# Optimization experiments

Measured on AMD Instinct MI355X. Metric: run time of the kernel, lower is better.

## Reference

```python
import jax, jax.numpy as jnp
import numpy as np

B = 2            # batch size
GRID = 256       # BEV grid H = W
M = 30000        # number of pillars (voxels)
NPTS = 200000    # number of points
IN_C = 16
VOXEL = 0.4      # voxel_size[:2]
PC_MIN = -51.2   # pc_range[:2]
DS = 2           # prod(ds_layer_strides)


def _bn(x, g, b):
    # eval-mode BatchNorm with running_mean=0, running_var=1 (eps absorbed into g)
    return x * g + b


def _conv(x, k, stride):
    # 3x3 conv, padding=1 (spconv SparseConv2d / SubMConv2d with pad k//2), NHWC
    return jax.lax.conv_general_dilated(
        x, k, (stride, stride), ((1, 1), (1, 1)),
        dimension_numbers=('NHWC', 'HWIO', 'NHWC'))


def _active_mask(occ, stride):
    # active output sites of a sparse conv = any active input in the 3x3 receptive field
    pooled = jax.lax.reduce_window(occ, -jnp.inf, jax.lax.max,
                                   (1, 3, 3, 1), (1, stride, stride, 1),
                                   ((0, 0), (1, 1), (1, 1), (0, 0)))
    return (pooled > 0).astype(occ.dtype)


def _forward(features, pfn_w0, pfn_g0, pfn_b0, pfn_w1, pfn_g1, pfn_b1,
             b1_kd, b1_gd, b1_bd, b1_k1, b1_g1, b1_b1, b1_k2, b1_g2, b1_b2,
             b2_kd, b2_gd, b2_bd, b2_k1, b2_g1, b2_b1, b2_k2, b2_g2, b2_b2,
             unq, unq_inv, grid_size):
    # pillar mode: cols 0:2 are xy; convert to (fractional) voxel coordinates
    pos = (features[:, :2] - PC_MIN) / VOXEL  # [N,2] = (px, py)

    # PFN layer 0 (not last): linear(16->16) + BN + ReLU, concat per-pillar max
    h = jax.nn.relu(_bn(features @ pfn_w0, pfn_g0, pfn_b0))            # [N,16]
    hmax = jax.ops.segment_max(h, unq_inv, num_segments=M)             # [M,16]
    h = jnp.concatenate([h, hmax[unq_inv]], axis=1)                    # [N,32]
    # PFN layer 1 (last): linear(32->64) + BN + ReLU
    h = jax.nn.relu(_bn(h @ pfn_w1, pfn_g1, pfn_b1))                   # [N,64]

    # scatter_max pooling points -> pillars
    fv = jax.ops.segment_max(h, unq_inv, num_segments=M)               # [M,64]

    Hn = grid_size
    img = jnp.zeros((B, Hn, Hn, fv.shape[1]), fv.dtype)
    img = img.at[unq[:, 0], unq[:, 1], unq[:, 2]].set(fv)              # dense BEV, NHWC
    occ = jnp.zeros((B, Hn, Hn, 1), fv.dtype)
    occ = occ.at[unq[:, 0], unq[:, 1], unq[:, 2]].set(1.0)

    # block 1: SparseConvBlock(stride=1) + SparseBasicBlock (dense math, masked to active sites)
    occ1 = _active_mask(occ, 1)
    x = jax.nn.relu(_bn(_conv(img, b1_kd, 1), b1_gd, b1_bd)) * occ1
    y = jax.nn.relu(_bn(_conv(x, b1_k1, 1), b1_g1, b1_b1)) * occ1
    y = _bn(_conv(y, b1_k2, 1), b1_g2, b1_b2) * occ1
    x = jax.nn.relu(x + y)

    # block 2: SparseConvBlock(stride=2) + SparseBasicBlock
    occ2 = _active_mask(occ1, 2)
    x = jax.nn.relu(_bn(_conv(x, b2_kd, 2), b2_gd, b2_bd)) * occ2
    y = jax.nn.relu(_bn(_conv(x, b2_k1, 1), b2_g1, b2_b1)) * occ2
    y = _bn(_conv(y, b2_k2, 1), b2_g2, b2_b2) * occ2
    x = jax.nn.relu(x + y)                                             # [B,H/2,W/2,128]

    # bilinear gather at per-point downsampled positions (px -> W axis, py -> H axis)
    bidx = unq[unq_inv, 0]
    px = pos[:, 0] / DS
    py = pos[:, 1] / DS
    Hc, Wc = x.shape[1], x.shape[2]
    x0 = jnp.clip(jnp.floor(px).astype(jnp.int32), 0, Wc - 1)
    x1 = jnp.clip(jnp.floor(px).astype(jnp.int32) + 1, 0, Wc - 1)
    y0 = jnp.clip(jnp.floor(py).astype(jnp.int32), 0, Hc - 1)
    y1 = jnp.clip(jnp.floor(py).astype(jnp.int32) + 1, 0, Hc - 1)
    Ia = x[bidx, y0, x0]
    Ib = x[bidx, y1, x0]
    Ic = x[bidx, y0, x1]
    Id = x[bidx, y1, x1]
    x0f, x1f = x0.astype(px.dtype), x1.astype(px.dtype)
    y0f, y1f = y0.astype(py.dtype), y1.astype(py.dtype)
    wa = ((x1f - px) * (y1f - py))[:, None]
    wb = ((x1f - px) * (py - y0f))[:, None]
    wc = ((px - x0f) * (y1f - py))[:, None]
    wd = ((px - x0f) * (py - y0f))[:, None]
    return Ia * wa + Ib * wb + Ic * wc + Id * wd                       # [N,128]


def setup_inputs() -> dict:
    rng = np.random.default_rng(0)
    d = {}
    d['features'] = jnp.asarray(rng.standard_normal((NPTS, IN_C)).astype(np.float32))
    # unique voxel coords (batch, y, x)
    lin = rng.choice(B * GRID * GRID, size=M, replace=False)
    d['unq'] = jnp.asarray(np.stack([lin // (GRID * GRID), (lin // GRID) % GRID, lin % GRID], 1).astype(np.int32))
    # every pillar gets at least one point
    d['unq_inv'] = jnp.asarray(np.concatenate([np.arange(M), rng.integers(0, M, NPTS - M)]).astype(np.int32))
    d['grid_size'] = GRID

    def w(*s):
        fan = int(np.prod(s[:-1]))
        return jnp.asarray((rng.standard_normal(s) / np.sqrt(fan)).astype(np.float32))

    def g(c):
        return jnp.asarray((0.5 + 0.5 * rng.random(c)).astype(np.float32))

    def bb(c):
        return jnp.asarray((0.1 * rng.standard_normal(c)).astype(np.float32))

    d['pfn_w0'] = w(IN_C, 16); d['pfn_g0'] = g(16); d['pfn_b0'] = bb(16)
    d['pfn_w1'] = w(32, 64);   d['pfn_g1'] = g(64); d['pfn_b1'] = bb(64)
    d['b1_kd'] = w(3, 3, 64, 64);   d['b1_gd'] = g(64);  d['b1_bd'] = bb(64)
    d['b1_k1'] = w(3, 3, 64, 64);   d['b1_g1'] = g(64);  d['b1_b1'] = bb(64)
    d['b1_k2'] = w(3, 3, 64, 64);   d['b1_g2'] = g(64);  d['b1_b2'] = bb(64)
    d['b2_kd'] = w(3, 3, 64, 128);  d['b2_gd'] = g(128); d['b2_bd'] = bb(128)
    d['b2_k1'] = w(3, 3, 128, 128); d['b2_g1'] = g(128); d['b2_b1'] = bb(128)
    d['b2_k2'] = w(3, 3, 128, 128); d['b2_g2'] = g(128); d['b2_b2'] = bb(128)
    return d


def reference(features, unq, unq_inv, grid_size,
              pfn_w0, pfn_g0, pfn_b0, pfn_w1, pfn_g1, pfn_b1,
              b1_kd, b1_gd, b1_bd, b1_k1, b1_g1, b1_b1, b1_k2, b1_g2, b1_b2,
              b2_kd, b2_gd, b2_bd, b2_k1, b2_g1, b2_b1, b2_k2, b2_g2, b2_b2):
    return _forward(features, pfn_w0, pfn_g0, pfn_b0, pfn_w1, pfn_g1, pfn_b1,
                    b1_kd, b1_gd, b1_bd, b1_k1, b1_g1, b1_b1, b1_k2, b1_g2, b1_b2,
                    b2_kd, b2_gd, b2_bd, b2_k1, b2_g1, b2_b1, b2_k2, b2_g2, b2_b2,
                    unq, unq_inv, grid_size)
```

## Files before the change

### kernel.cpp

```cpp
#include <hip/hip_runtime.h>
#include <hip/hip_bf16.h>

#define NPTS    200000
#define MPIL    30000
#define BATCH   2
#define GRID0   256
#define PCMIN   (-51.2f)
#define VOXEL0  (0.4f)
#define NCHUNK  118

#define SLOT_B  ((size_t)16777216)
#define SLOT_F  ((size_t)33554432)

#define W0F 0
#define W1F 256
#define FB1 9216
#define FB2 156672
#define FB3 304128
#define FB4 451584
#define FB5 746496
#define FB6 1336320

#define WS_FLAG 0
#define WS_OCC8 64
#define WS_OCC1 (64 + 131072)
#define WS_OCC2 (64 + 262144)
#define WS_HMAX 393280
#define WS_CNT  2313280
#define WS_OFF  2433280
#define WS_CUR  2553344
#define WS_IDX  2673344
#define WS_LOC  3473344
#define WS_BS   3593344
#define WS_FX   393344

typedef __attribute__((ext_vector_type(8))) short v8s;
typedef __attribute__((ext_vector_type(4))) float f32x4;

static __device__ __forceinline__ float b2f(__hip_bfloat16 v) { return __bfloat162float(v); }
static __device__ __forceinline__ unsigned short f2bbits(float f) {
    __hip_bfloat16 h = __float2bfloat16(f);
    union { __hip_bfloat16 h; unsigned short u; } cv; cv.h = h; return cv.u;
}
static __device__ __forceinline__ float bits2f(unsigned short h) {
    union { unsigned int u; float f; } c; c.u = ((unsigned int)h) << 16; return c.f;
}
static __device__ __forceinline__ float lo2f(unsigned int u) {
    union { unsigned int u; float f; } c; c.u = u << 16; return c.f;
}
static __device__ __forceinline__ float hi2f(unsigned int u) {
    union { unsigned int u; float f; } c; c.u = u & 0xFFFF0000u; return c.f;
}
static __device__ __forceinline__ unsigned int pack2(float a, float b) {
    return (unsigned int)f2bbits(a) | ((unsigned int)f2bbits(b) << 16);
}
static __device__ __forceinline__ void split2(float a, float b, unsigned int& hi, unsigned int& lo) {
    unsigned short ha = f2bbits(a), hb = f2bbits(b);
    hi = (unsigned int)ha | ((unsigned int)hb << 16);
    float ra = a - bits2f(ha);
    float rb = b - bits2f(hb);
    lo = (unsigned int)f2bbits(ra) | ((unsigned int)f2bbits(rb) << 16);
}

static __device__ __forceinline__ float ldf(const void* p, size_t i, int isb) {
    return isb ? b2f(((const __hip_bfloat16*)p)[i]) : ((const float*)p)[i];
}
static __device__ __forceinline__ float4 ld4(const void* p, size_t i, int isb) {
    if (isb) {
        uint2 r = *(const uint2*)((const __hip_bfloat16*)p + i);
        return make_float4(lo2f(r.x), hi2f(r.x), lo2f(r.y), hi2f(r.y));
    }
    return *(const float4*)((const float*)p + i);
}
static __device__ __forceinline__ void st4(void* p, size_t i, int isb, float4 v) {
    if (isb) {
        uint2 pk; pk.x = pack2(v.x, v.y); pk.y = pack2(v.z, v.w);
        *(uint2*)((__hip_bfloat16*)p + i) = pk;
    } else {
        *(float4*)((float*)p + i) = v;
    }
}
static __device__ __forceinline__ void* actptr(void* ob, int slot, int isb) {
    return (char*)ob + (size_t)slot * (isb ? SLOT_B : SLOT_F);
}
static __device__ __forceinline__ float* wpool(void* ob, int isb) {
    return (float*)((char*)ob + 3 * (isb ? SLOT_B : SLOT_F));
}

__global__ void probe_kernel(const unsigned short* __restrict__ g0, int* __restrict__ flag) {
    if (threadIdx.x == 0 && blockIdx.x == 0) {
        int ok = 1;
        for (int i = 0; i < 8; i++) {
            unsigned short u = g0[i];
            if (u < 0x3E00 || u >= 0x4000) ok = 0;
        }
        *flag = ok;
    }
}

__global__ __launch_bounds__(256) void cvt_kernel(const void* __restrict__ src, void* ob,
                                                  int woff, int n, const int* __restrict__ flag) {
    int isb = *flag;
    int i = blockIdx.x * 256 + threadIdx.x;
    if (i < n) wpool(ob, isb)[woff + i] = ldf(src, i, isb);
}

__global__ __launch_bounds__(256) void wfrag_kernel(const void* __restrict__ src, void* ob,
                                                    int fb_bytes, int CIN, int COUT,
                                                    const int* __restrict__ flag)
{
    const int isb = *flag;
    const int cnt = 9 * CIN * COUT;
    int e = blockIdx.x * 256 + threadIdx.x;
    if (e >= cnt) return;
    int i = e & 7;
    int l = (e >> 3) & 63;
    int f = e >> 9;
    int nbn = COUT >> 4, kcn = CIN >> 5;
    int nb = f % nbn;
    int kc = (f / nbn) % kcn;
    int tap = f / (nbn * kcn);
    int ci = kc * 32 + (l >> 4) * 8 + i;
    int co = nb * 16 + (l & 15);
    float wv = ldf(src, (size_t)(tap * CIN + ci) * COUT + co, isb);
    unsigned short h = f2bbits(wv);
    float rem = wv - bits2f(h);
    short* wh = (short*)((char*)ob + 3 * (isb ? SLOT_B : SLOT_F) + fb_bytes);
    wh[e] = (short)h;
    wh[cnt + e] = (short)f2bbits(rem);
}

__global__ __launch_bounds__(256) void hist_kernel(const int* __restrict__ unq_inv,
                                                   int* __restrict__ cnt)
{
    int n = blockIdx.x * 256 + threadIdx.x;
    if (n < NPTS) atomicAdd(&cnt[unq_inv[n]], 1);
}

__global__ __launch_bounds__(256) void scan1_kernel(const int* __restrict__ cnt,
                                                    int* __restrict__ loc,
                                                    int* __restrict__ bs)
{
    __shared__ int s[256];
    const int tid = threadIdx.x;
    const int i = blockIdx.x * 256 + tid;
    int v = (i < MPIL) ? cnt[i] : 0;
    s[tid] = v;
    __syncthreads();
#pragma unroll
    for (int d = 1; d < 256; d <<= 1) {
        int t = (tid >= d) ? s[tid - d] : 0;
        __syncthreads();
        s[tid] += t;
        __syncthreads();
    }
    if (i < MPIL) loc[i] = s[tid] - v;
    if (tid == 255) bs[blockIdx.x] = s[255];
}

__global__ __launch_bounds__(128) void scan2_kernel(int* __restrict__ bs)
{
    __shared__ int s[NCHUNK];
    const int tid = threadIdx.x;
    for (int i = tid; i < NCHUNK; i += 128) s[i] = bs[i];
    __syncthreads();
    if (tid == 0) {
        int acc = 0;
        for (int i = 0; i < NCHUNK; i++) { int t = s[i]; s[i] = acc; acc += t; }
    }
    __syncthreads();
    for (int i = tid; i < NCHUNK; i += 128) bs[i] = s[i];
}

__global__ __launch_bounds__(256) void scan3_kernel(const int* __restrict__ loc,
                                                    const int* __restrict__ bs,
                                                    int* __restrict__ off,
                                                    int* __restrict__ cur)
{
    int i = blockIdx.x * 256 + threadIdx.x;
    if (i < MPIL) {
        int e = loc[i] + bs[blockIdx.x];
        off[i] = e; cur[i] = e;
    }
    if (i == 0) off[MPIL] = NPTS;
}

__global__ __launch_bounds__(256) void fill_kernel(const int* __restrict__ unq_inv,
                                                   int* __restrict__ cur,
                                                   int* __restrict__ idxarr)
{
    int n = blockIdx.x * 256 + threadIdx.x;
    if (n >= NPTS) return;
    int p = unq_inv[n];
    int s = atomicAdd(&cur[p], 1);
    idxarr[s] = n;
}

__global__ __launch_bounds__(256) void pfn0_kernel(
    const void* __restrict__ feat, void* ob, const void* __restrict__ g0,
    const void* __restrict__ b0, const int* __restrict__ flag)
{
    const int isb = *flag;
    int n = blockIdx.x * 256 + threadIdx.x;
    if (n >= NPTS) return;
    const float* w0f = wpool(ob, isb) + W0F;
    void* h0 = actptr(ob, 1, isb);
    float f[16];
#pragma unroll
    for (int i = 0; i < 16; i += 4) {
        float4 v = ld4(feat, (size_t)n * 16 + i, isb);
        f[i] = v.x; f[i + 1] = v.y; f[i + 2] = v.z; f[i + 3] = v.w;
    }
#pragma unroll
    for (int co = 0; co < 16; co += 4) {
        float a0 = 0.f, a1 = 0.f, a2 = 0.f, a3 = 0.f;
#pragma unroll
        for (int ci = 0; ci < 16; ci++) {
            float4 w = *(const float4*)&w0f[ci * 16 + co];
            a0 += f[ci] * w.x; a1 += f[ci] * w.y; a2 += f[ci] * w.z; a3 += f[ci] * w.w;
        }
        float o[4] = { a0, a1, a2, a3 };
#pragma unroll
        for (int k = 0; k < 4; k++) {
            float z = o[k] * ldf(g0, co + k, isb) + ldf(b0, co + k, isb);
            o[k] = fmaxf(z, 0.f);
        }
        st4(h0, (size_t)n * 16 + co, isb, make_float4(o[0], o[1], o[2], o[3]));
    }
}

__global__ __launch_bounds__(256) void hmax_kernel(
    void* ob, const int* __restrict__ off, const int* __restrict__ idxarr,
    float* __restrict__ hmax, const int* __restrict__ flag)
{
    const int isb = *flag;
    int t = blockIdx.x * 256 + threadIdx.x;
    if (t >= MPIL * 16) return;
    int p = t >> 4, ch = t & 15;
    const void* h0 = actptr(ob, 1, isb);
    float m = 0.f;
    int s1 = off[p + 1];
    for (int s = off[p]; s < s1; s++) {
        int n = idxarr[s];
        m = fmaxf(m, ldf(h0, (size_t)n * 16 + ch, isb));
    }
    hmax[t] = m;
}

template<bool BF>
static __device__ __forceinline__ void pfn1p_body(
    void* ob, const float* __restrict__ hmax, const void* __restrict__ g1,
    const void* __restrict__ b1, const int* __restrict__ off,
    const int* __restrict__ idxarr, const int* __restrict__ unq,
    unsigned char* __restrict__ occ)
{
    const int lane = threadIdx.x & 63;
    const int p = (blockIdx.x << 2) + (threadIdx.x >> 6);
    if (p >= MPIL) return;
    const int isb = BF ? 1 : 0;
    const float* w1f = wpool(ob, isb) + W1F;
    const void* h0 = actptr(ob, 1, isb);
    void* img = actptr(ob, 0, isb);

    float wcol[32];
#pragma unroll
    for (int k = 0; k < 32; k++) wcol[k] = w1f[k * 64 + lane];
    float base = 0.f;
#pragma unroll
    for (int k = 0; k < 16; k++) base += hmax[(size_t)p * 16 + k] * wcol[16 + k];
    const float g = ldf(g1, lane, isb);
    const float be = ldf(b1, lane, isb);

    float m = 0.f;
    const int s1 = off[p + 1];
    for (int s = off[p]; s < s1; s++) {
        const int n = idxarr[s];
        float h[16];
        if (BF) {
            const unsigned short* hp = (const unsigned short*)h0 + (size_t)n * 16;
            uint4 a = *(const uint4*)hp;
            uint4 c = *(const uint4*)(hp + 8);
            h[0] = lo2f(a.x); h[1] = hi2f(a.x); h[2] = lo2f(a.y); h[3] = hi2f(a.y);
            h[4] = lo2f(a.z); h[5] = hi2f(a.z); h[6] = lo2f(a.w); h[7] = hi2f(a.w);
            h[8] = lo2f(c.x); h[9] = hi2f(c.x); h[10] = lo2f(c.y); h[11] = hi2f(c.y);
            h[12] = lo2f(c.z); h[13] = hi2f(c.z); h[14] = lo2f(c.w); h[15] = hi2f(c.w);
        } else {
            const float* fp = (const float*)h0 + (size_t)n * 16;
#pragma unroll
            for (int i = 0; i < 16; i += 4) {
                float4 v = *(const float4*)(fp + i);
                h[i] = v.x; h[i + 1] = v.y; h[i + 2] = v.z; h[i + 3] = v.w;
            }
        }
        float z = base;
#pragma unroll
        for (int k = 0; k < 16; k++) z += h[k] * wcol[k];
        z = fmaxf(z * g + be, 0.f);
        m = fmaxf(m, z);
    }

    const int bb = unq[p * 3 + 0], yy = unq[p * 3 + 1], xx = unq[p * 3 + 2];
    const size_t site = ((size_t)bb * GRID0 + yy) * GRID0 + xx;
    if (BF) ((unsigned short*)img)[site * 64 + lane] = f2bbits(m);
    else    ((float*)img)[site * 64 + lane] = m;
    if (lane == 0) occ[site] = 1;
}

__global__ __launch_bounds__(256) void pfn1p_kernel(
    void* ob, const float* __restrict__ hmax, const void* __restrict__ g1,
    const void* __restrict__ b1, const int* __restrict__ off,
    const int* __restrict__ idxarr, const int* __restrict__ unq,
    unsigned char* __restrict__ occ, const int* __restrict__ flag)
{
    if (*flag) pfn1p_body<true>(ob, hmax, g1, b1, off, idxarr, unq, occ);
    else       pfn1p_body<false>(ob, hmax, g1, b1, off, idxarr, unq, occ);
}

__global__ __launch_bounds__(256) void dilate1_kernel(const unsigned char* __restrict__ occ,
                                                      unsigned char* __restrict__ occ1)
{
    int idx = blockIdx.x * 256 + threadIdx.x;
    if (idx >= BATCH * GRID0 * GRID0) return;
    int b = idx / (GRID0 * GRID0);
    int r = idx % (GRID0 * GRID0);
    int y = r / GRID0, x = r % GRID0;
    unsigned char v = 0;
#pragma unroll
    for (int dy = -1; dy <= 1; dy++) {
        int yy = y + dy; if (yy < 0 || yy >= GRID0) continue;
#pragma unroll
        for (int dx = -1; dx <= 1; dx++) {
            int xx = x + dx; if (xx < 0 || xx >= GRID0) continue;
            v |= occ[((size_t)b * GRID0 + yy) * GRID0 + xx];
        }
    }
    occ1[idx] = v ? 1 : 0;
}

__global__ __launch_bounds__(256) void dilate2_kernel(const unsigned char* __restrict__ occ1,
                                                      unsigned char* __restrict__ occ2)
{
    int idx = blockIdx.x * 256 + threadIdx.x;
    if (idx >= BATCH * 128 * 128) return;
    int b = idx / (128 * 128);
    int r = idx % (128 * 128);
    int y = r / 128, x = r % 128;
    unsigned char v = 0;
#pragma unroll
    for (int dy = -1; dy <= 1; dy++) {
        int yy = 2 * y + dy; if (yy < 0 || yy >= GRID0) continue;
#pragma unroll
        for (int dx = -1; dx <= 1; dx++) {
            int xx = 2 * x + dx; if (xx < 0 || xx >= GRID0) continue;
            v |= occ1[((size_t)b * GRID0 + yy) * GRID0 + xx];
        }
    }
    occ2[idx] = v ? 1 : 0;
}

template<int CIN, int COUT, int STRIDE, bool ADD_RES, bool BF, int RT, int WR, int WC>
static __device__ __forceinline__ void conv_tile(
    short* s_a, const void* in, void* outp, const void* res, const short* wh,
    const void* gamma, const void* beta, const unsigned char* mask,
    int HIN, int WIN, int HOUT, int WOUT, int b, int oy0, int ox0, int nbB)
{
    constexpr int Y_EXT = (RT - 1) * STRIDE + 3;
    constexpr int X_EXT = 15 * STRIDE + 3;
    constexpr int PSTR = CIN + 8;
    constexpr int TSZ = Y_EXT * X_EXT * PSTR;
    constexpr int NCH8 = CIN / 8;
    constexpr int RRW = RT / WR;
    constexpr int NBW = COUT / 16 / 2 / WC;
    constexpr int KCN = CIN / 32;
    constexpr int NOB = COUT / 16;

    const int tid = threadIdx.x;

    __syncthreads();
    for (int i = tid; i < Y_EXT * X_EXT * NCH8; i += 256) {
        int c8 = i % NCH8;
        int r = i / NCH8;
        int xo = r % X_EXT;
        int dy = r / X_EXT;
        int yin = oy0 * STRIDE - 1 + dy;
        int xin = ox0 * STRIDE - 1 + xo;
        bool inb = (yin >= 0 && yin < HIN && xin >= 0 && xin < WIN);
        int si = (dy * X_EXT + xo) * PSTR + c8 * 8;
        size_t gi = (((size_t)b * HIN + yin) * WIN + xin) * (size_t)CIN + c8 * 8;
        if (BF) {
            uint4 v = make_uint4(0u, 0u, 0u, 0u);
            if (inb) v = *(const uint4*)((const unsigned short*)in + gi);
            *(uint4*)&s_a[si] = v;
        } else {
            float4 va = make_float4(0.f, 0.f, 0.f, 0.f);
            float4 vb = make_float4(0.f, 0.f, 0.f, 0.f);
            if (inb) {
                va = *(const float4*)((const float*)in + gi);
                vb = *(const float4*)((const float*)in + gi + 4);
            }
            uint4 hv, lv;
            split2(va.x, va.y, hv.x, lv.x);
            split2(va.z, va.w, hv.y, lv.y);
            split2(vb.x, vb.y, hv.z, lv.z);
            split2(vb.z, vb.w, hv.w, lv.w);
            *(uint4*)&s_a[si] = hv;
            *(uint4*)&s_a[TSZ + si] = lv;
        }
    }
    __syncthreads();

    const int lane = tid & 63;
    const int w = tid >> 6;
    const int wr = w / WC;
    const int wn = w % WC;
    const int nb0 = nbB + wn * NBW;
    const int row0 = wr * RRW;
    const int l15 = lane & 15;
    const int lhi = lane >> 4;
    const short* wl = wh + 9 * CIN * COUT;

    f32x4 acc[RRW][NBW];
#pragma unroll
    for (int rr = 0; rr < RRW; rr++)
#pragma unroll
        for (int nb = 0; nb < NBW; nb++) acc[rr][nb] = (f32x4){0.f, 0.f, 0.f, 0.f};

#pragma unroll 1
    for (int tap = 0; tap < 9; tap++) {
        const int ky = tap / 3;
        const int kx = tap - ky * 3;
        const int axy = ky * X_EXT + l15 * STRIDE + kx;
#pragma unroll
        for (int kc = 0; kc < KCN; kc++) {
            const int f0 = (tap * KCN + kc) * NOB + nb0;
            v8s bh[NBW];
#pragma unroll
            for (int nb = 0; nb < NBW; nb++)
                bh[nb] = *(const v8s*)&wh[(size_t)(f0 + nb) * 512 + lane * 8];
#pragma unroll
            for (int rr = 0; rr < RRW; rr++) {
                const int abase = ((row0 + rr) * STRIDE * X_EXT + axy) * PSTR + lhi * 8 + kc * 32;
                const v8s ah = *(const v8s*)&s_a[abase];
#pragma unroll
                for (int nb = 0; nb < NBW; nb++)
                    acc[rr][nb] = __builtin_amdgcn_mfma_f32_16x16x32_bf16(ah, bh[nb], acc[rr][nb], 0, 0, 0);
                if constexpr (!BF) {
                    const v8s al = *(const v8s*)&s_a[TSZ + abase];
#pragma unroll
                    for (int nb = 0; nb < NBW; nb++) {
                        const v8s bl = *(const v8s*)&wl[(size_t)(f0 + nb) * 512 + lane * 8];
                        acc[rr][nb] = __builtin_amdgcn_mfma_f32_16x16x32_bf16(ah, bl, acc[rr][nb], 0, 0, 0);
                        acc[rr][nb] = __builtin_amdgcn_mfma_f32_16x16x32_bf16(al, bh[nb], acc[rr][nb], 0, 0, 0);
                    }
                }
            }
        }
    }

#pragma unroll
    for (int rr = 0; rr < RRW; rr++) {
        const int oy = oy0 + row0 + rr;
        const size_t mrow = ((size_t)b * HOUT + oy) * WOUT + ox0 + lhi * 4;
        const unsigned int mw = *(const unsigned int*)&mask[mrow];
#pragma unroll
        for (int nb = 0; nb < NBW; nb++) {
            const int n = (nb0 + nb) * 16 + l15;
            const float g = ldf(gamma, n, BF ? 1 : 0);
            const float be = ldf(beta, n, BF ? 1 : 0);
#pragma unroll
            for (int r = 0; r < 4; r++) {
                const size_t oaddr = (mrow + r) * COUT + n;
                float z = acc[rr][nb][r] * g + be;
                z *= ((mw >> (8 * r)) & 0xFF) ? 1.f : 0.f;
                if constexpr (ADD_RES) z += ldf(res, oaddr, BF ? 1 : 0);
                z = fmaxf(z, 0.f);
                if (BF) ((unsigned short*)outp)[oaddr] = f2bbits(z);
                else    ((float*)outp)[oaddr] = z;
            }
        }
    }
}

template<int CIN, int COUT, int STRIDE, int R, int RTF, int WR, int WC, bool ADD_RES>
__global__ __launch_bounds__(256) void convmf_kernel(
    void* ob, int in_slot, int out_slot, void* out_ws, int res_slot, int fb_bytes,
    const void* __restrict__ gamma, const void* __restrict__ beta,
    const unsigned char* __restrict__ mask, const int* __restrict__ flag,
    int HIN, int WIN, int HOUT, int WOUT)
{
    constexpr int X_EXT = 15 * STRIDE + 3;
    constexpr int PSTR = CIN + 8;
    constexpr int TSZ_B = ((R - 1) * STRIDE + 3) * X_EXT * PSTR;
    constexpr int TSZ_F = ((RTF - 1) * STRIDE + 3) * X_EXT * PSTR;
    constexpr int LDS_SH = (TSZ_B > 2 * TSZ_F) ? TSZ_B : 2 * TSZ_F;
    __shared__ __align__(16) short s_a[LDS_SH];

    const int nbx = gridDim.x, nby = gridDim.y;
    const int nwg = nbx * nby * (int)gridDim.z;
    int bid = blockIdx.x + nbx * (blockIdx.y + nby * blockIdx.z);
    bid = (bid & 7) * (nwg >> 3) + (bid >> 3);
    const int bx = bid % nbx;
    const int byy = (bid / nbx) % nby;
    const int bzz = bid / (nbx * nby);
    const int b = bzz >> 1;
    const int coh = bzz & 1;
    const int nbB = coh * (COUT / 32);

    const int isb = *flag;
    const void* in = actptr(ob, in_slot, isb);
    void* outp = out_ws ? out_ws : actptr(ob, out_slot, isb);
    const void* res = ADD_RES ? actptr(ob, res_slot, isb) : nullptr;
    const short* wh = (const short*)((const char*)ob + 3 * (isb ? SLOT_B : SLOT_F) + fb_bytes);

    if (isb) {
        conv_tile<CIN, COUT, STRIDE, ADD_RES, true, R, WR, WC>(
            s_a, in, outp, res, wh, gamma, beta, mask,
            HIN, WIN, HOUT, WOUT, b, byy * R, bx * 16, nbB);
    } else {
#pragma unroll
        for (int p = 0; p < R / RTF; p++)
            conv_tile<CIN, COUT, STRIDE, ADD_RES, false, RTF, WR, WC>(
                s_a, in, outp, res, wh, gamma, beta, mask,
                HIN, WIN, HOUT, WOUT, b, byy * R + p * RTF, bx * 16, nbB);
    }
}

__global__ __launch_bounds__(256) void gather_kernel(
    const void* __restrict__ x, const void* __restrict__ feat,
    const int* __restrict__ unq, const int* __restrict__ unq_inv,
    void* __restrict__ out, const int* __restrict__ flag)
{
    const int isb = *flag;
    int idx = blockIdx.x * 256 + threadIdx.x;
    if (idx >= NPTS * 32) return;
    int n = idx >> 5;
    int co = (idx & 31) * 4;
    float fx = ldf(feat, (size_t)n * 16 + 0, isb);
    float fy = ldf(feat, (size_t)n * 16 + 1, isb);
    float px = ((fx - PCMIN) / VOXEL0) / 2.0f;
    float py = ((fy - PCMIN) / VOXEL0) / 2.0f;
    int bi = unq[(size_t)unq_inv[n] * 3 + 0];
    int xf = (int)floorf(px), yf = (int)floorf(py);
    int x0 = min(max(xf, 0), 127), x1 = min(max(xf + 1, 0), 127);
    int y0 = min(max(yf, 0), 127), y1 = min(max(yf + 1, 0), 127);
    float x0f = (float)x0, x1f = (float)x1, y0f = (float)y0, y1f = (float)y1;
    float wa = (x1f - px) * (y1f - py);
    float wb = (x1f - px) * (py - y0f);
    float wc = (px - x0f) * (y1f - py);
    float wd = (px - x0f) * (py - y0f);
    size_t base = (size_t)bi * 128 * 128 * 128;
    float4 Ia = ld4(x, base + ((size_t)y0 * 128 + x0) * 128 + co, isb);
    float4 Ib = ld4(x, base + ((size_t)y1 * 128 + x0) * 128 + co, isb);
    float4 Ic = ld4(x, base + ((size_t)y0 * 128 + x1) * 128 + co, isb);
    float4 Id = ld4(x, base + ((size_t)y1 * 128 + x1) * 128 + co, isb);
    float4 r;
    r.x = Ia.x * wa + Ib.x * wb + Ic.x * wc + Id.x * wd;
    r.y = Ia.y * wa + Ib.y * wb + Ic.y * wc + Id.y * wd;
    r.z = Ia.z * wa + Ib.z * wb + Ic.z * wc + Id.z * wd;
    r.w = Ia.w * wa + Ib.w * wb + Ic.w * wc + Id.w * wd;
    st4(out, (size_t)n * 128 + co, isb, r);
}

extern "C" void kernel_launch(void* const* d_in, const int* in_sizes, int n_in,
                              void* d_out, int out_size, void* d_ws, size_t ws_size,
                              hipStream_t stream)
{
    (void)in_sizes; (void)n_in; (void)out_size; (void)ws_size;
    const int* unq = (const int*)d_in[1];
    const int* unq_inv = (const int*)d_in[2];

    char* ws = (char*)d_ws;
    int* flagp = (int*)(ws + WS_FLAG);
    unsigned char* occ8 = (unsigned char*)(ws + WS_OCC8);
    unsigned char* occ1m = (unsigned char*)(ws + WS_OCC1);
    unsigned char* occ2m = (unsigned char*)(ws + WS_OCC2);
    float* hmax = (float*)(ws + WS_HMAX);
    int* cnt = (int*)(ws + WS_CNT);
    int* off = (int*)(ws + WS_OFF);
    int* cur = (int*)(ws + WS_CUR);
    int* idxarr = (int*)(ws + WS_IDX);
    int* loc = (int*)(ws + WS_LOC);
    int* bs = (int*)(ws + WS_BS);
    void* Fx = (void*)(ws + WS_FX);

    probe_kernel<<<1, 64, 0, stream>>>((const unsigned short*)d_in[5], flagp);

    cvt_kernel<<<1, 256, 0, stream>>>(d_in[4], d_out, W0F, 256, flagp);
    cvt_kernel<<<8, 256, 0, stream>>>(d_in[7], d_out, W1F, 2048, flagp);
    wfrag_kernel<<<144, 256, 0, stream>>>(d_in[10], d_out, FB1, 64, 64, flagp);
    wfrag_kernel<<<144, 256, 0, stream>>>(d_in[13], d_out, FB2, 64, 64, flagp);
    wfrag_kernel<<<144, 256, 0, stream>>>(d_in[16], d_out, FB3, 64, 64, flagp);
    wfrag_kernel<<<288, 256, 0, stream>>>(d_in[19], d_out, FB4, 64, 128, flagp);
    wfrag_kernel<<<576, 256, 0, stream>>>(d_in[22], d_out, FB5, 128, 128, flagp);
    wfrag_kernel<<<576, 256, 0, stream>>>(d_in[25], d_out, FB6, 128, 128, flagp);

    hipMemsetAsync(d_out, 0, SLOT_F, stream);
    hipMemsetAsync(cnt, 0, (size_t)MPIL * 4, stream);
    hipMemsetAsync(occ8, 0, 131072, stream);

    hist_kernel<<<(NPTS + 255) / 256, 256, 0, stream>>>(unq_inv, cnt);
    scan1_kernel<<<NCHUNK, 256, 0, stream>>>(cnt, loc, bs);
    scan2_kernel<<<1, 128, 0, stream>>>(bs);
    scan3_kernel<<<NCHUNK, 256, 0, stream>>>(loc, bs, off, cur);
    fill_kernel<<<(NPTS + 255) / 256, 256, 0, stream>>>(unq_inv, cur, idxarr);
    pfn0_kernel<<<(NPTS + 255) / 256, 256, 0, stream>>>(d_in[0], d_out, d_in[5], d_in[6], flagp);
    hmax_kernel<<<(MPIL * 16 + 255) / 256, 256, 0, stream>>>(d_out, off, idxarr, hmax, flagp);
    pfn1p_kernel<<<(MPIL + 3) / 4, 256, 0, stream>>>(d_out, hmax, d_in[8], d_in[9],
                                                     off, idxarr, unq, occ8, flagp);

    dilate1_kernel<<<(BATCH * GRID0 * GRID0) / 256, 256, 0, stream>>>(occ8, occ1m);
    dilate2_kernel<<<(BATCH * 128 * 128) / 256, 256, 0, stream>>>(occ1m, occ2m);

    dim3 blk(256);
    dim3 g1(16, 32, BATCH * 2);
    convmf_kernel<64, 64, 1, 8, 2, 2, 2, false><<<g1, blk, 0, stream>>>(
        d_out, 0, 1, nullptr, 0, FB1, d_in[11], d_in[12], occ1m, flagp, 256, 256, 256, 256);
    convmf_kernel<64, 64, 1, 8, 2, 2, 2, false><<<g1, blk, 0, stream>>>(
        d_out, 1, 2, nullptr, 0, FB2, d_in[14], d_in[15], occ1m, flagp, 256, 256, 256, 256);
    convmf_kernel<64, 64, 1, 8, 2, 2, 2, true><<<g1, blk, 0, stream>>>(
        d_out, 2, 0, nullptr, 1, FB3, d_in[17], d_in[18], occ1m, flagp, 256, 256, 256, 256);
    dim3 g2a(8, 64, BATCH * 2), g2b(8, 32, BATCH * 2);
    convmf_kernel<64, 128, 2, 2, 1, 1, 4, false><<<g2a, blk, 0, stream>>>(
        d_out, 0, 1, nullptr, 0, FB4, d_in[20], d_in[21], occ2m, flagp, 256, 256, 128, 128);
    convmf_kernel<128, 128, 1, 4, 1, 1, 4, false><<<g2b, blk, 0, stream>>>(
        d_out, 1, 2, nullptr, 0, FB5, d_in[23], d_in[24], occ2m, flagp, 128, 128, 128, 128);
    convmf_kernel<128, 128, 1, 4, 1, 1, 4, true><<<g2b, blk, 0, stream>>>(
        d_out, 2, 0, Fx, 1, FB6, d_in[26], d_in[27], occ2m, flagp, 128, 128, 128, 128);

    gather_kernel<<<(NPTS * 32) / 256, 256, 0, stream>>>(Fx, d_in[0], unq, unq_inv,
                                                         d_out, flagp);
}
```

Before: 640.9 us.

## Restructure MFMA conv tiles: swap operands, XOR-swizzle LDS, batch weight loads

The implicit-GEMM conv tile now puts weights in the A operand and activations in the B operand. Each lane therefore owns four consecutive output channels, which allows vectorized epilogue stores and residual loads. LDS padding is replaced by an XOR swizzle on 8-channel groups to avoid bank conflicts, and weight fragments for several K-chunks are preloaded per pass to hide global latency. Block 1 convs drop the output-channel split so each block covers all 64 channels, and warp layouts change, at the cost of higher register pressure and fewer workgroups.

Measured after the change: 563.6 us. 1.14x faster.

```diff
diff --git a/kernel.cpp b/kernel.cpp
--- a/kernel.cpp
+++ b/kernel.cpp
@@ -358,7 +358,7 @@
     occ2[idx] = v ? 1 : 0;
 }
 
-template<int CIN, int COUT, int STRIDE, bool ADD_RES, bool BF, int RT, int WR, int WC>
+template<int CIN, int COUT, int STRIDE, bool ADD_RES, bool BF, int RT, int WC, int WP, int CSPLIT>
 static __device__ __forceinline__ void conv_tile(
     short* s_a, const void* in, void* outp, const void* res, const short* wh,
     const void* gamma, const void* beta, const unsigned char* mask,
@@ -366,12 +366,14 @@
 {
     constexpr int Y_EXT = (RT - 1) * STRIDE + 3;
     constexpr int X_EXT = 15 * STRIDE + 3;
-    constexpr int PSTR = CIN + 8;
-    constexpr int TSZ = Y_EXT * X_EXT * PSTR;
+    constexpr int TSZ = Y_EXT * X_EXT * CIN;
     constexpr int NCH8 = CIN / 8;
-    constexpr int RRW = RT / WR;
-    constexpr int NBW = COUT / 16 / 2 / WC;
+    constexpr int RPW = RT / WP;
+    constexpr int CG = COUT / 16 / CSPLIT / WC;
     constexpr int KCN = CIN / 32;
+    constexpr int KCNT = 9 * KCN;
+    constexpr int CP = BF ? 9 : 3;
+    constexpr int NPASS = KCNT / CP;
     constexpr int NOB = COUT / 16;
 
     const int tid = threadIdx.x;
@@ -385,7 +387,7 @@
         int yin = oy0 * STRIDE - 1 + dy;
         int xin = ox0 * STRIDE - 1 + xo;
         bool inb = (yin >= 0 && yin < HIN && xin >= 0 && xin < WIN);
-        int si = (dy * X_EXT + xo) * PSTR + c8 * 8;
+        int si = (dy * X_EXT + xo) * CIN + ((c8 ^ (xo & 7)) << 3);
         size_t gi = (((size_t)b * HIN + yin) * WIN + xin) * (size_t)CIN + c8 * 8;
         if (BF) {
             uint4 v = make_uint4(0u, 0u, 0u, 0u);
@@ -411,46 +413,53 @@
 
     const int lane = tid & 63;
     const int w = tid >> 6;
-    const int wr = w / WC;
-    const int wn = w % WC;
-    const int nb0 = nbB + wn * NBW;
-    const int row0 = wr * RRW;
+    const int cgb = nbB + (w % WC) * CG;
+    const int row0 = (w / WC) * RPW;
     const int l15 = lane & 15;
     const int lhi = lane >> 4;
     const short* wl = wh + 9 * CIN * COUT;
 
-    f32x4 acc[RRW][NBW];
-#pragma unroll
-    for (int rr = 0; rr < RRW; rr++)
-#pragma unroll
-        for (int nb = 0; nb < NBW; nb++) acc[rr][nb] = (f32x4){0.f, 0.f, 0.f, 0.f};
+    f32x4 acc[RPW][CG];
+#pragma unroll
+    for (int pt = 0; pt < RPW; pt++)
+#pragma unroll
+        for (int g = 0; g < CG; g++) acc[pt][g] = (f32x4){0.f, 0.f, 0.f, 0.f};
 
 #pragma unroll 1
-    for (int tap = 0; tap < 9; tap++) {
-        const int ky = tap / 3;
-        const int kx = tap - ky * 3;
-        const int axy = ky * X_EXT + l15 * STRIDE + kx;
-#pragma unroll
-        for (int kc = 0; kc < KCN; kc++) {
-            const int f0 = (tap * KCN + kc) * NOB + nb0;
-            v8s bh[NBW];
-#pragma unroll
-            for (int nb = 0; nb < NBW; nb++)
-                bh[nb] = *(const v8s*)&wh[(size_t)(f0 + nb) * 512 + lane * 8];
-#pragma unroll
-            for (int rr = 0; rr < RRW; rr++) {
-                const int abase = ((row0 + rr) * STRIDE * X_EXT + axy) * PSTR + lhi * 8 + kc * 32;
-                const v8s ah = *(const v8s*)&s_a[abase];
-#pragma unroll
-                for (int nb = 0; nb < NBW; nb++)
-                    acc[rr][nb] = __builtin_amdgcn_mfma_f32_16x16x32_bf16(ah, bh[nb], acc[rr][nb], 0, 0, 0);
+    for (int ps = 0; ps < NPASS; ps++) {
+        const int cb0 = ps * CP;
+        v8s wa[CP * CG];
+        v8s wo[BF ? 1 : CP * CG];
+#pragma unroll
+        for (int c = 0; c < CP; c++)
+#pragma unroll
+            for (int g = 0; g < CG; g++) {
+                const size_t f = (size_t)(cb0 + c) * NOB + cgb + g;
+                wa[c * CG + g] = *(const v8s*)&wh[f * 512 + lane * 8];
+                if constexpr (!BF)
+                    wo[c * CG + g] = *(const v8s*)&wl[f * 512 + lane * 8];
+            }
+#pragma unroll
+        for (int c = 0; c < CP; c++) {
+            const int cgl = cb0 + c;
+            const int tap = cgl / KCN;
+            const int kc = cgl - tap * KCN;
+            const int ky = tap / 3, kx = tap - ky * 3;
+            const int xo = l15 * STRIDE + kx;
+            const int coff = (((kc * 4 + lhi) ^ (xo & 7)) << 3);
+#pragma unroll
+            for (int pt = 0; pt < RPW; pt++) {
+                const int ba = (((row0 + pt) * STRIDE + ky) * X_EXT + xo) * CIN + coff;
+                const v8s bv = *(const v8s*)&s_a[ba];
+#pragma unroll
+                for (int g = 0; g < CG; g++)
+                    acc[pt][g] = __builtin_amdgcn_mfma_f32_16x16x32_bf16(wa[c * CG + g], bv, acc[pt][g], 0, 0, 0);
                 if constexpr (!BF) {
-                    const v8s al = *(const v8s*)&s_a[TSZ + abase];
-#pragma unroll
-                    for (int nb = 0; nb < NBW; nb++) {
-                        const v8s bl = *(const v8s*)&wl[(size_t)(f0 + nb) * 512 + lane * 8];
-                        acc[rr][nb] = __builtin_amdgcn_mfma_f32_16x16x32_bf16(ah, bl, acc[rr][nb], 0, 0, 0);
-                        acc[rr][nb] = __builtin_amdgcn_mfma_f32_16x16x32_bf16(al, bh[nb], acc[rr][nb], 0, 0, 0);
+                    const v8s bl = *(const v8s*)&s_a[TSZ + ba];
+#pragma unroll
+                    for (int g = 0; g < CG; g++) {
+                        acc[pt][g] = __builtin_amdgcn_mfma_f32_16x16x32_bf16(wa[c * CG + g], bl, acc[pt][g], 0, 0, 0);
+                        acc[pt][g] = __builtin_amdgcn_mfma_f32_16x16x32_bf16(wo[c * CG + g], bv, acc[pt][g], 0, 0, 0);
                     }
                 }
             }
@@ -458,30 +467,48 @@
     }
 
 #pragma unroll
-    for (int rr = 0; rr < RRW; rr++) {
-        const int oy = oy0 + row0 + rr;
-        const size_t mrow = ((size_t)b * HOUT + oy) * WOUT + ox0 + lhi * 4;
-        const unsigned int mw = *(const unsigned int*)&mask[mrow];
-#pragma unroll
-        for (int nb = 0; nb < NBW; nb++) {
-            const int n = (nb0 + nb) * 16 + l15;
-            const float g = ldf(gamma, n, BF ? 1 : 0);
-            const float be = ldf(beta, n, BF ? 1 : 0);
-#pragma unroll
-            for (int r = 0; r < 4; r++) {
-                const size_t oaddr = (mrow + r) * COUT + n;
-                float z = acc[rr][nb][r] * g + be;
-                z *= ((mw >> (8 * r)) & 0xFF) ? 1.f : 0.f;
-                if constexpr (ADD_RES) z += ldf(res, oaddr, BF ? 1 : 0);
-                z = fmaxf(z, 0.f);
-                if (BF) ((unsigned short*)outp)[oaddr] = f2bbits(z);
-                else    ((float*)outp)[oaddr] = z;
+    for (int g = 0; g < CG; g++) {
+        const int ch = (cgb + g) * 16 + lhi * 4;
+        float gm[4], bt[4];
+#pragma unroll
+        for (int r = 0; r < 4; r++) {
+            gm[r] = ldf(gamma, ch + r, BF ? 1 : 0);
+            bt[r] = ldf(beta, ch + r, BF ? 1 : 0);
+        }
+#pragma unroll
+        for (int pt = 0; pt < RPW; pt++) {
+            const int oy = oy0 + row0 + pt;
+            const size_t prow = ((size_t)b * HOUT + oy) * WOUT + ox0 + l15;
+            const float mk = mask[prow] ? 1.f : 0.f;
+            float z[4];
+#pragma unroll
+            for (int r = 0; r < 4; r++)
+                z[r] = (acc[pt][g][r] * gm[r] + bt[r]) * mk;
+            if constexpr (ADD_RES) {
+                if (BF) {
+                    uint2 rr = *(const uint2*)((const unsigned short*)res + prow * COUT + ch);
+                    z[0] += lo2f(rr.x); z[1] += hi2f(rr.x);
+                    z[2] += lo2f(rr.y); z[3] += hi2f(rr.y);
+                } else {
+                    float4 rr = *(const float4*)((const float*)res + prow * COUT + ch);
+                    z[0] += rr.x; z[1] += rr.y; z[2] += rr.z; z[3] += rr.w;
+                }
             }
-        }
-    }
-}
-
-template<int CIN, int COUT, int STRIDE, int R, int RTF, int WR, int WC, bool ADD_RES>
+#pragma unroll
+            for (int r = 0; r < 4; r++) z[r] = fmaxf(z[r], 0.f);
+            if (BF) {
+                uint2 pk;
+                pk.x = pack2(z[0], z[1]);
+                pk.y = pack2(z[2], z[3]);
+                *(uint2*)((unsigned short*)outp + prow * COUT + ch) = pk;
+            } else {
+                *(float4*)((float*)outp + prow * COUT + ch) = make_float4(z[0], z[1], z[2], z[3]);
+            }
+        }
+    }
+}
+
+template<int CIN, int COUT, int STRIDE, int R, int RTF, int CSPLIT, bool ADD_RES>
 __global__ __launch_bounds__(256) void convmf_kernel(
     void* ob, int in_slot, int out_slot, void* out_ws, int res_slot, int fb_bytes,
     const void* __restrict__ gamma, const void* __restrict__ beta,
@@ -489,10 +516,9 @@
     int HIN, int WIN, int HOUT, int WOUT)
 {
     constexpr int X_EXT = 15 * STRIDE + 3;
-    constexpr int PSTR = CIN + 8;
-    constexpr int TSZ_B = ((R - 1) * STRIDE + 3) * X_EXT * PSTR;
-    constexpr int TSZ_F = ((RTF - 1) * STRIDE + 3) * X_EXT * PSTR;
-    constexpr int LDS_SH = (TSZ_B > 2 * TSZ_F) ? TSZ_B : 2 * TSZ_F;
+    constexpr int TSZ_B = ((R - 1) * STRIDE + 3) * X_EXT * CIN;
+    constexpr int TSZ_F2 = 2 * (((RTF - 1) * STRIDE + 3) * X_EXT * CIN);
+    constexpr int LDS_SH = (TSZ_B > TSZ_F2) ? TSZ_B : TSZ_F2;
     __shared__ __align__(16) short s_a[LDS_SH];
 
     const int nbx = gridDim.x, nby = gridDim.y;
@@ -502,9 +528,9 @@
     const int bx = bid % nbx;
     const int byy = (bid / nbx) % nby;
     const int bzz = bid / (nbx * nby);
-    const int b = bzz >> 1;
-    const int coh = bzz & 1;
-    const int nbB = coh * (COUT / 32);
+    const int b = bzz / CSPLIT;
+    const int coh = bzz % CSPLIT;
+    const int nbB = coh * (COUT / 16 / CSPLIT);
 
     const int isb = *flag;
     const void* in = actptr(ob, in_slot, isb);
@@ -513,13 +539,13 @@
     const short* wh = (const short*)((const char*)ob + 3 * (isb ? SLOT_B : SLOT_F) + fb_bytes);
 
     if (isb) {
-        conv_tile<CIN, COUT, STRIDE, ADD_RES, true, R, WR, WC>(
+        conv_tile<CIN, COUT, STRIDE, ADD_RES, true, R, 2, 2, CSPLIT>(
             s_a, in, outp, res, wh, gamma, beta, mask,
             HIN, WIN, HOUT, WOUT, b, byy * R, bx * 16, nbB);
     } else {
-#pragma unroll
+#pragma unroll 1
         for (int p = 0; p < R / RTF; p++)
-            conv_tile<CIN, COUT, STRIDE, ADD_RES, false, RTF, WR, WC>(
+            conv_tile<CIN, COUT, STRIDE, ADD_RES, false, RTF, 4, 1, CSPLIT>(
                 s_a, in, outp, res, wh, gamma, beta, mask,
                 HIN, WIN, HOUT, WOUT, b, byy * R + p * RTF, bx * 16, nbB);
     }
@@ -612,19 +638,19 @@
     dilate2_kernel<<<(BATCH * 128 * 128) / 256, 256, 0, stream>>>(occ1m, occ2m);
 
     dim3 blk(256);
-    dim3 g1(16, 32, BATCH * 2);
-    convmf_kernel<64, 64, 1, 8, 2, 2, 2, false><<<g1, blk, 0, stream>>>(
+    dim3 g1(16, 32, BATCH);
+    convmf_kernel<64, 64, 1, 8, 2, 1, false><<<g1, blk, 0, stream>>>(
         d_out, 0, 1, nullptr, 0, FB1, d_in[11], d_in[12], occ1m, flagp, 256, 256, 256, 256);
-    convmf_kernel<64, 64, 1, 8, 2, 2, 2, false><<<g1, blk, 0, stream>>>(
+    convmf_kernel<64, 64, 1, 8, 2, 1, false><<<g1, blk, 0, stream>>>(
         d_out, 1, 2, nullptr, 0, FB2, d_in[14], d_in[15], occ1m, flagp, 256, 256, 256, 256);
-    convmf_kernel<64, 64, 1, 8, 2, 2, 2, true><<<g1, blk, 0, stream>>>(
+    convmf_kernel<64, 64, 1, 8, 2, 1, true><<<g1, blk, 0, stream>>>(
         d_out, 2, 0, nullptr, 1, FB3, d_in[17], d_in[18], occ1m, flagp, 256, 256, 256, 256);
     dim3 g2a(8, 64, BATCH * 2), g2b(8, 32, BATCH * 2);
-    convmf_kernel<64, 128, 2, 2, 1, 1, 4, false><<<g2a, blk, 0, stream>>>(
+    convmf_kernel<64, 128, 2, 2, 1, 2, false><<<g2a, blk, 0, stream>>>(
         d_out, 0, 1, nullptr, 0, FB4, d_in[20], d_in[21], occ2m, flagp, 256, 256, 128, 128);
-    convmf_kernel<128, 128, 1, 4, 1, 1, 4, false><<<g2b, blk, 0, stream>>>(
+    convmf_kernel<128, 128, 1, 4, 1, 2, false><<<g2b, blk, 0, stream>>>(
         d_out, 1, 2, nullptr, 0, FB5, d_in[23], d_in[24], occ2m, flagp, 128, 128, 128, 128);
-    convmf_kernel<128, 128, 1, 4, 1, 1, 4, true><<<g2b, blk, 0, stream>>>(
+    convmf_kernel<128, 128, 1, 4, 1, 2, true><<<g2b, blk, 0, stream>>>(
         d_out, 2, 0, Fx, 1, FB6, d_in[26], d_in[27], occ2m, flagp, 128, 128, 128, 128);
 
     gather_kernel<<<(NPTS * 32) / 256, 256, 0, stream>>>(Fx, d_in[0], unq, unq_inv,
```
